# Optimization experiments

Measured on AMD Instinct MI355X. Metric: run time of the kernel, lower is better.

The kernel has to match this reference:

```python
import jax, jax.numpy as jnp
import numpy as np

N_NODES = 50000
N_EDGES = 1600000
IN_DIM = 128
HEADS = 4
OUT_DIM = 32
LEAKY_SLOPE = 0.2
BETA = 0.5
C = 1.2


def setup_inputs() -> dict:
    key = jax.random.key(0)
    k1, k2, k3, k4, k5, k6 = jax.random.split(key, 6)
    x = jax.random.normal(k1, (N_NODES, IN_DIM), dtype=jnp.float32)
    edge_index = jax.random.randint(k2, (2, N_EDGES), 0, N_NODES, dtype=jnp.int64)
    # GATConv params: shared linear (no bias), per-head attention vectors, output bias
    glorot = 1.0 / np.sqrt(IN_DIM)
    W = jax.random.uniform(k3, (IN_DIM, HEADS * OUT_DIM), jnp.float32, -glorot, glorot)
    att_src = jax.random.uniform(k4, (HEADS, OUT_DIM), jnp.float32, -glorot, glorot)
    att_dst = jax.random.uniform(k5, (HEADS, OUT_DIM), jnp.float32, -glorot, glorot)
    bias = jnp.zeros((HEADS * OUT_DIM,), jnp.float32)
    return {"x": x, "edge_index": edge_index, "W": W,
            "att_src": att_src, "att_dst": att_dst, "bias": bias}


def reference(x, edge_index, W, att_src, att_dst, bias):
    N = x.shape[0]
    H, D = att_src.shape
    # add self loops (edge j->i aggregates at i)
    loop = jnp.arange(N, dtype=edge_index.dtype)
    src = jnp.concatenate([edge_index[0], loop])  # [Etot]
    dst = jnp.concatenate([edge_index[1], loop])
    # per-head projection
    xp = (x @ W).reshape(N, H, D)                 # [N,H,D]
    a_src = jnp.einsum('nhd,hd->nh', xp, att_src)  # [N,H]
    a_dst = jnp.einsum('nhd,hd->nh', xp, att_dst)
    alpha = jax.nn.leaky_relu(a_src[src] + a_dst[dst], LEAKY_SLOPE)  # [Etot,H]
    # scatter-softmax over incoming edges per target node (self loops ensure coverage)
    amax = jax.ops.segment_max(alpha, dst, num_segments=N)
    e = jnp.exp(alpha - amax[dst])
    denom = jax.ops.segment_sum(e, dst, num_segments=N)
    w = e / (denom[dst] + 1e-16)                  # [Etot,H]
    # weighted scatter-add aggregation
    msg = xp[src] * w[:, :, None]                 # [Etot,H,D]
    out = jax.ops.segment_sum(msg, dst, num_segments=N).reshape(N, H * D)
    z = out + bias
    # beta-mix Swish (non-learnable swish beta = 1)
    return BETA * z + (C - BETA) * (z * jax.nn.sigmoid(z))
```

## Files before the change

kernel.cpp:

```cpp
#include <hip/hip_runtime.h>
#include <hip/hip_bf16.h>
#include <hip/hip_fp16.h>
#include <stdint.h>

#define LEAKY 0.2f
#define MIX_BETA 0.5f
#define MIX_C 1.2f

#define FBITS 7
#define FSZ   (1 << FBITS)
#define NBMX  512
#define CH    4096
#define EPT   16
#define CAPP  5632

using short8 = __attribute__((ext_vector_type(8))) short;
using f32x4  = __attribute__((ext_vector_type(4))) float;

__device__ __forceinline__ unsigned f2bf(float f) {
    unsigned u = __float_as_uint(f);
    return (u + 0x7fffu + ((u >> 16) & 1u)) >> 16;
}
__device__ __forceinline__ unsigned pack2bf(float a, float b) {
    return f2bf(a) | (f2bf(b) << 16);
}
__device__ __forceinline__ float hlo(unsigned u) {
    return __half2float(__ushort_as_half((uint16_t)(u & 0xFFFFu)));
}
__device__ __forceinline__ float hhi(unsigned u) {
    return __half2float(__ushort_as_half((uint16_t)(u >> 16)));
}
__device__ __forceinline__ float leaky_exp(float v) {
    v = fmaxf(v, LEAKY * v);
    return __expf(v);
}

__global__ __launch_bounds__(512) void k_prep(const void* x, const void* ei, const void* W,
                                              const void* att_s, const void* att_d,
                                              const void* bias, int N, int* flags,
                                              float* att_sf, float* att_df, float* biasf,
                                              uint16_t* Wtg, int* gbcursor) {
    __shared__ uint16_t wt[128][136];
    __shared__ int lf[2];
    const int t = threadIdx.x;
    if (t < NBMX) gbcursor[t] = 0;
    if (t < 64) {
        const uint16_t* u = (const uint16_t*)x;
        uint16_t v = u[2 * t];
        int ef = (v >> 7) & 0xFF;
        bool ok = (ef >= 90 && ef <= 140);
        unsigned long long all_ok = __ballot(ok);
        const unsigned long long* e64 = (const unsigned long long*)ei;
        bool big = (e64[t] >= (unsigned long long)N);
        unsigned long long anybig = __ballot(big);
        if (t == 0) {
            int f0 = (all_ok == ~0ull) ? 1 : 0;
            int f1 = (anybig != 0ull) ? 1 : 0;
            flags[0] = f0; flags[1] = f1;
            lf[0] = f0; lf[1] = f1;
        }
    }
    __syncthreads();
    const bool bf = lf[0] != 0;
    if (t >= 64 && t < 448) {
        int i = t - 64;
        const void* in; float* out; int idx;
        if (i < 128)      { in = att_s; out = att_sf; idx = i; }
        else if (i < 256) { in = att_d; out = att_df; idx = i - 128; }
        else              { in = bias;  out = biasf;  idx = i - 256; }
        float v = bf ? __uint_as_float(((unsigned)((const uint16_t*)in)[idx]) << 16)
                     : ((const float*)in)[idx];
        out[idx] = v;
    }
    for (int s = t; s < 4096; s += 512) {
        int k = s >> 5, c4 = (s & 31) * 4;
        ushort4 hv;
        if (bf) {
            hv = *(const ushort4*)((const uint16_t*)W + k * 128 + c4);
        } else {
            float4 v = *(const float4*)((const float*)W + k * 128 + c4);
            hv.x = (uint16_t)f2bf(v.x); hv.y = (uint16_t)f2bf(v.y);
            hv.z = (uint16_t)f2bf(v.z); hv.w = (uint16_t)f2bf(v.w);
        }
        wt[c4 + 0][k] = hv.x; wt[c4 + 1][k] = hv.y;
        wt[c4 + 2][k] = hv.z; wt[c4 + 3][k] = hv.w;
    }
    __syncthreads();
    for (int s = t; s < 2048; s += 512) {
        int r = s >> 4, ch = (s & 15) * 8;
        *(int4*)(Wtg + r * 128 + ch) = *(const int4*)&wt[r][ch];
    }
}

__global__ __launch_bounds__(256) void k_mid(const void* x, const void* ei,
                                             const uint16_t* Wtg,
                                             const float* att_sf, const float* att_df,
                                             const int* flags, int N, int E, int G,
                                             int nb, int cap, int* gbcursor,
                                             unsigned* entries,
                                             unsigned* xph, float* a_src, float* a_dst) {
    __shared__ char smem[40960] __attribute__((aligned(16)));
    const int t = threadIdx.x;

    if ((int)blockIdx.x < G) {
        uint16_t (*xs)[136]  = (uint16_t(*)[136])smem;
        float (*asrc_t)[4]   = (float(*)[4])(smem + 34816);
        float (*adst_t)[4]   = (float(*)[4])(smem + 36864);
        const bool bf = flags[0] != 0;
        const int row0 = blockIdx.x * 128;

        for (int s = t; s < 4096; s += 256) {
            int r = s >> 5, kc = (s & 31) * 4;
            int rr = row0 + r; if (rr >= N) rr = N - 1;
            size_t g = (size_t)rr * 128 + kc;
            ushort4 hv;
            if (bf) {
                hv = *(const ushort4*)((const uint16_t*)x + g);
            } else {
                float4 v = *(const float4*)((const float*)x + g);
                hv.x = (uint16_t)f2bf(v.x); hv.y = (uint16_t)f2bf(v.y);
                hv.z = (uint16_t)f2bf(v.z); hv.w = (uint16_t)f2bf(v.w);
            }
            *(ushort4*)&xs[r][kc] = hv;
        }
        __syncthreads();

        const int w = t >> 6, l = t & 63;
        const int rA = l & 15;
        const int kg = (l >> 4) * 8;
        f32x4 acc[2][8];
#pragma unroll
        for (int fr = 0; fr < 2; ++fr)
#pragma unroll
            for (int fc = 0; fc < 8; ++fc) acc[fr][fc] = (f32x4){0.f, 0.f, 0.f, 0.f};

#pragma unroll
        for (int kk = 0; kk < 4; ++kk) {
            const int kb = kk * 32 + kg;
            short8 a0 = *(const short8*)&xs[w * 32 + rA][kb];
            short8 a1 = *(const short8*)&xs[w * 32 + 16 + rA][kb];
            const uint16_t* wp = Wtg + rA * 128 + kb;
#pragma unroll
            for (int fc = 0; fc < 8; ++fc) {
                short8 b = *(const short8*)(wp + fc * 2048);
                acc[0][fc] = __builtin_amdgcn_mfma_f32_16x16x32_bf16(a0, b, acc[0][fc], 0, 0, 0);
                acc[1][fc] = __builtin_amdgcn_mfma_f32_16x16x32_bf16(a1, b, acc[1][fc], 0, 0, 0);
            }
        }
        __syncthreads();

#pragma unroll
        for (int fr = 0; fr < 2; ++fr)
#pragma unroll
            for (int fc = 0; fc < 8; ++fc) {
                int row = w * 32 + fr * 16 + (l >> 4) * 4;
                int col = fc * 16 + rA;
#pragma unroll
                for (int j = 0; j < 4; ++j)
                    xs[row + j][col] = __half_as_ushort(__float2half(acc[fr][fc][j]));
            }
        __syncthreads();

        for (int s = t; s < 2048; s += 256) {
            int r = s >> 4, ch = (s & 15) * 8;
            int rr = row0 + r;
            if (rr < N)
                *(int4*)((uint16_t*)xph + (size_t)rr * 128 + ch) = *(const int4*)&xs[r][ch];
        }
        for (int s = t; s < 512; s += 256) {
            int r = s >> 2, hh = s & 3;
            int rr = row0 + r;
            if (rr < N) {
                float ss = 0.f, sd = 0.f;
#pragma unroll
                for (int q = 0; q < 32; ++q) {
                    float v = __half2float(__ushort_as_half(xs[r][hh * 32 + q]));
                    ss = fmaf(v, att_sf[hh * 32 + q], ss);
                    sd = fmaf(v, att_df[hh * 32 + q], sd);
                }
                a_src[(size_t)rr * 4 + hh] = ss;
                a_dst[(size_t)rr * 4 + hh] = sd;
            }
        }
    } else {
        unsigned* st  = (unsigned*)smem;
        uint16_t* bb  = (uint16_t*)(smem + 16384);
        int* lcnt     = (int*)(smem + 24576);
        int* loff     = (int*)(smem + 26624);
        int* lbase    = (int*)(smem + 28672);
        int* wcur     = (int*)(smem + 30720);
        int* sc       = (int*)(smem + 32768);
        const bool is32 = flags[1] != 0;
        const int chunk0 = ((int)blockIdx.x - G) * CH;
        const int nvalid = min(CH, E - chunk0);

        int se[EPT], de[EPT];
        lcnt[t] = 0; lcnt[t + 256] = 0;
        wcur[t] = 0; wcur[t + 256] = 0;
        __syncthreads();
#pragma unroll
        for (int k = 0; k < EPT; ++k) {
            int i = chunk0 + k * 256 + t;
            if (i < E) {
                int s, d;
                if (is32) { const int* p = (const int*)ei; s = p[i]; d = p[E + i]; }
                else { const long long* p = (const long long*)ei; s = (int)p[i]; d = (int)p[E + i]; }
                se[k] = s; de[k] = d;
                atomicAdd(&lcnt[d >> FBITS], 1);
            } else {
                de[k] = -1;
            }
        }
        __syncthreads();
        sc[t] = lcnt[2 * t] + lcnt[2 * t + 1];
        __syncthreads();
        for (int o = 1; o < 256; o <<= 1) {
            int v = (t >= o) ? sc[t - o] : 0;
            __syncthreads();
            sc[t] += v;
            __syncthreads();
        }
        {
            int excl = (t > 0) ? sc[t - 1] : 0;
            int k0 = 2 * t, k1 = 2 * t + 1;
            loff[k0] = excl;
            loff[k1] = excl + lcnt[k0];
#pragma unroll
            for (int q = 0; q < 2; ++q) {
                int k = k0 + q;
                if (k < nb && lcnt[k]) {
                    int m = min(lcnt[k], cap);
                    int base = atomicAdd(&gbcursor[k], lcnt[k]);
                    if (base > cap - m) base = cap - m;
                    if (base < 0) base = 0;
                    lbase[k] = base;
                }
            }
        }
        __syncthreads();
#pragma unroll
        for (int k = 0; k < EPT; ++k) {
            int d = de[k];
            if (d >= 0) {
                int b = d >> FBITS;
                int slot = atomicAdd(&wcur[b], 1);
                int pos = loff[b] + slot;
                st[pos] = (unsigned)se[k] | ((unsigned)(d & (FSZ - 1)) << 17);
                bb[pos] = (uint16_t)b;
            }
        }
        __syncthreads();
        for (int s = t; s < nvalid; s += 256) {
            int b = bb[s];
            int pos = lbase[b] + (s - loff[b]);
            if (pos >= 0 && pos < cap)
                entries[(size_t)b * cap + pos] = st[s];
        }
    }
}

__global__ __launch_bounds__(1024) void k_final(const unsigned* entries, const int* gbcursor,
                                                int cap, int N,
                                                const float* a_src, const float* a_dst,
                                                const unsigned* xph, const float* biasf,
                                                const int* flags, void* out) {
    __shared__ uint16_t ssrc_l[CAPP];
    __shared__ __half   ews_l[(CAPP / 4) * 16];
    __shared__ int ncnt[FSZ], nscan[FSZ], wcur[FSZ], poff[FSZ];
    const int b = blockIdx.x;
    const int t = threadIdx.x;
    const int node0 = b << FBITS;
    const size_t eb = (size_t)b * cap;
    const int count = min(gbcursor[b], cap);

    for (int i = t; i < CAPP / 2; i += 1024) ((unsigned*)ssrc_l)[i] = 0u;
    for (int i = t; i < (CAPP / 4) * 8; i += 1024) ((unsigned*)ews_l)[i] = 0u;
    if (t < FSZ) ncnt[t] = 0;
    __syncthreads();
    for (int i = t; i < count; i += 1024)
        atomicAdd(&ncnt[entries[eb + i] >> 17], 1);
    __syncthreads();
    if (t < FSZ) nscan[t] = (ncnt[t] + 3) & ~3;
    __syncthreads();
    for (int o = 1; o < FSZ; o <<= 1) {
        int v = (t < FSZ && t >= o) ? nscan[t - o] : 0;
        __syncthreads();
        if (t < FSZ) nscan[t] += v;
        __syncthreads();
    }
    if (t < FSZ) {
        int pcnt = (ncnt[t] + 3) & ~3;
        int px = nscan[t] - pcnt;
        wcur[t] = px;
        poff[t] = px;
    }
    __syncthreads();
    for (int i = t; i < count; i += 1024) {
        unsigned e = entries[eb + i];
        int dlo = (int)(e >> 17);
        int s = (int)(e & 0x1FFFFu);
        int slot = atomicAdd(&wcur[dlo], 1);
        if (slot < CAPP) {
            int d = node0 + dlo;
            float4 as = *(const float4*)(a_src + (size_t)s * 4);
            float4 ad = *(const float4*)(a_dst + (size_t)d * 4);
            float e0 = leaky_exp(as.x + ad.x);
            float e1 = leaky_exp(as.y + ad.y);
            float e2 = leaky_exp(as.z + ad.z);
            float e3 = leaky_exp(as.w + ad.w);
            ssrc_l[slot] = (uint16_t)s;
            __half* pe = &ews_l[(slot >> 2) * 16];
            int j = slot & 3;
            pe[j]      = __float2half(e0);
            pe[4 + j]  = __float2half(e1);
            pe[8 + j]  = __float2half(e2);
            pe[12 + j] = __float2half(e3);
        }
    }
    __syncthreads();

    const int wv = t >> 6, lane = t & 63;
    const int hi = lane >> 5;
    const int l = lane & 31;
    const int d0 = l * 4;
    const int h = l >> 3;
    const char* xb = (const char*)xph;
    const int outbf = flags[0];

    for (int k = wv; k < FSZ / 2; k += 16) {
        int ln = 2 * k + hi;
        int n = node0 + ln;
        bool ok = n < N;
        int nn = ok ? n : (N - 1);
        int nc = ok ? ncnt[ln] : 0;

        float adst = a_dst[(size_t)nn * 4 + h];
        float e = leaky_exp(a_src[(size_t)nn * 4 + h] + adst);
        uint2 xw = *(const uint2*)(xb + (size_t)nn * 256 + d0 * 2);
        float4 acc;
        acc.x = e * hlo(xw.x); acc.y = e * hhi(xw.x);
        acc.z = e * hlo(xw.y); acc.w = e * hhi(xw.y);
        float den = e;

        const int beg = ok ? poff[ln] : 0;
        const int gb = beg >> 2;
        const int ng = (nc + 3) >> 2;
        int g = 0;
        for (; g + 2 <= ng; g += 2) {
            ushort4 s4a = *(const ushort4*)&ssrc_l[beg + 4 * g];
            ushort4 s4b = *(const ushort4*)&ssrc_l[beg + 4 * g + 4];
            uint2 ea = *(const uint2*)&ews_l[(gb + g) * 16 + h * 4];
            uint2 ebw = *(const uint2*)&ews_l[(gb + g + 1) * 16 + h * 4];
            uint2 w0 = *(const uint2*)(xb + (size_t)s4a.x * 256 + d0 * 2);
            uint2 w1 = *(const uint2*)(xb + (size_t)s4a.y * 256 + d0 * 2);
            uint2 w2 = *(const uint2*)(xb + (size_t)s4a.z * 256 + d0 * 2);
            uint2 w3 = *(const uint2*)(xb + (size_t)s4a.w * 256 + d0 * 2);
            uint2 w4 = *(const uint2*)(xb + (size_t)s4b.x * 256 + d0 * 2);
            uint2 w5 = *(const uint2*)(xb + (size_t)s4b.y * 256 + d0 * 2);
            uint2 w6 = *(const uint2*)(xb + (size_t)s4b.z * 256 + d0 * 2);
            uint2 w7 = *(const uint2*)(xb + (size_t)s4b.w * 256 + d0 * 2);
            float e0 = hlo(ea.x), e1 = hhi(ea.x), e2 = hlo(ea.y), e3 = hhi(ea.y);
            float e4 = hlo(ebw.x), e5 = hhi(ebw.x), e6 = hlo(ebw.y), e7 = hhi(ebw.y);
            acc.x = fmaf(e0, hlo(w0.x), acc.x); acc.y = fmaf(e0, hhi(w0.x), acc.y);
            acc.z = fmaf(e0, hlo(w0.y), acc.z); acc.w = fmaf(e0, hhi(w0.y), acc.w);
            acc.x = fmaf(e1, hlo(w1.x), acc.x); acc.y = fmaf(e1, hhi(w1.x), acc.y);
            acc.z = fmaf(e1, hlo(w1.y), acc.z); acc.w = fmaf(e1, hhi(w1.y), acc.w);
            acc.x = fmaf(e2, hlo(w2.x), acc.x); acc.y = fmaf(e2, hhi(w2.x), acc.y);
            acc.z = fmaf(e2, hlo(w2.y), acc.z); acc.w = fmaf(e2, hhi(w2.y), acc.w);
            acc.x = fmaf(e3, hlo(w3.x), acc.x); acc.y = fmaf(e3, hhi(w3.x), acc.y);
            acc.z = fmaf(e3, hlo(w3.y), acc.z); acc.w = fmaf(e3, hhi(w3.y), acc.w);
            acc.x = fmaf(e4, hlo(w4.x), acc.x); acc.y = fmaf(e4, hhi(w4.x), acc.y);
            acc.z = fmaf(e4, hlo(w4.y), acc.z); acc.w = fmaf(e4, hhi(w4.y), acc.w);
            acc.x = fmaf(e5, hlo(w5.x), acc.x); acc.y = fmaf(e5, hhi(w5.x), acc.y);
            acc.z = fmaf(e5, hlo(w5.y), acc.z); acc.w = fmaf(e5, hhi(w5.y), acc.w);
            acc.x = fmaf(e6, hlo(w6.x), acc.x); acc.y = fmaf(e6, hhi(w6.x), acc.y);
            acc.z = fmaf(e6, hlo(w6.y), acc.z); acc.w = fmaf(e6, hhi(w6.y), acc.w);
            acc.x = fmaf(e7, hlo(w7.x), acc.x); acc.y = fmaf(e7, hhi(w7.x), acc.y);
            acc.z = fmaf(e7, hlo(w7.y), acc.z); acc.w = fmaf(e7, hhi(w7.y), acc.w);
            den += ((e0 + e1) + (e2 + e3)) + ((e4 + e5) + (e6 + e7));
        }
        if (g < ng) {
            ushort4 s4 = *(const ushort4*)&ssrc_l[beg + 4 * g];
            uint2 ea = *(const uint2*)&ews_l[(gb + g) * 16 + h * 4];
            float e0 = hlo(ea.x), e1 = hhi(ea.x), e2 = hlo(ea.y), e3 = hhi(ea.y);
            uint2 w0 = *(const uint2*)(xb + (size_t)s4.x * 256 + d0 * 2);
            uint2 w1 = *(const uint2*)(xb + (size_t)s4.y * 256 + d0 * 2);
            uint2 w2 = *(const uint2*)(xb + (size_t)s4.z * 256 + d0 * 2);
            uint2 w3 = *(const uint2*)(xb + (size_t)s4.w * 256 + d0 * 2);
            acc.x = fmaf(e0, hlo(w0.x), acc.x); acc.y = fmaf(e0, hhi(w0.x), acc.y);
            acc.z = fmaf(e0, hlo(w0.y), acc.z); acc.w = fmaf(e0, hhi(w0.y), acc.w);
            acc.x = fmaf(e1, hlo(w1.x), acc.x); acc.y = fmaf(e1, hhi(w1.x), acc.y);
            acc.z = fmaf(e1, hlo(w1.y), acc.z); acc.w = fmaf(e1, hhi(w1.y), acc.w);
            acc.x = fmaf(e2, hlo(w2.x), acc.x); acc.y = fmaf(e2, hhi(w2.x), acc.y);
            acc.z = fmaf(e2, hlo(w2.y), acc.z); acc.w = fmaf(e2, hhi(w2.y), acc.w);
            acc.x = fmaf(e3, hlo(w3.x), acc.x); acc.y = fmaf(e3, hhi(w3.x), acc.y);
            acc.z = fmaf(e3, hlo(w3.y), acc.z); acc.w = fmaf(e3, hhi(w3.y), acc.w);
            den += (e0 + e1) + (e2 + e3);
        }
        float inv = 1.f / (den + 1e-16f);
        float4 bv = *(const float4*)(biasf + d0);
        float z0 = fmaf(acc.x, inv, bv.x);
        float z1 = fmaf(acc.y, inv, bv.y);
        float z2 = fmaf(acc.z, inv, bv.z);
        float z3 = fmaf(acc.w, inv, bv.w);
        float r0 = MIX_BETA * z0 + (MIX_C - MIX_BETA) * z0 / (1.f + __expf(-z0));
        float r1 = MIX_BETA * z1 + (MIX_C - MIX_BETA) * z1 / (1.f + __expf(-z1));
        float r2 = MIX_BETA * z2 + (MIX_C - MIX_BETA) * z2 / (1.f + __expf(-z2));
        float r3 = MIX_BETA * z3 + (MIX_C - MIX_BETA) * z3 / (1.f + __expf(-z3));
        if (ok) {
            if (outbf) {
                uint2 ov = make_uint2(pack2bf(r0, r1), pack2bf(r2, r3));
                *(uint2*)((uint16_t*)out + (size_t)n * 128 + d0) = ov;
            } else {
                *(float4*)((float*)out + (size_t)n * 128 + d0) = make_float4(r0, r1, r2, r3);
            }
        }
    }
}

extern "C" void kernel_launch(void* const* d_in, const int* in_sizes, int n_in,
                              void* d_out, int out_size, void* d_ws, size_t ws_size,
                              hipStream_t stream) {
    const void* x     = d_in[0];
    const void* ei    = d_in[1];
    const void* W     = d_in[2];
    const void* att_s = d_in[3];
    const void* att_d = d_in[4];
    const void* bias  = d_in[5];
    const int N = in_sizes[0] / 128;
    const int E = in_sizes[1] / 2;
    const int NB = (N + FSZ - 1) >> FBITS;
    int cap = E / NB + E / (8 * NB) + 512;
    const int capmax = CAPP - 3 * FSZ - 8;
    if (cap > capmax) cap = capmax;

    char* ws = (char*)d_ws;
    size_t off = 0;
    auto alloc = [&](size_t bytes) -> void* {
        void* p = ws + off;
        off += (bytes + 255) & ~(size_t)255;
        return p;
    };
    int* flags        = (int*)alloc(16);
    unsigned* entries = (unsigned*)alloc((size_t)NB * cap * 4);
    int* gbcursor     = (int*)alloc(NBMX * 4);
    unsigned* xph     = (unsigned*)alloc((size_t)N * 64 * 4);
    float* a_src      = (float*)alloc((size_t)N * 4 * 4);
    float* a_dst      = (float*)alloc((size_t)N * 4 * 4);
    float* att_sf     = (float*)alloc(128 * 4);
    float* att_df     = (float*)alloc(128 * 4);
    float* biasf      = (float*)alloc(128 * 4);
    uint16_t* Wtg     = (uint16_t*)alloc(128 * 128 * 2);

    const int G = (N + 127) / 128;
    const int S = (E + CH - 1) / CH;

    k_prep<<<1, 512, 0, stream>>>(x, ei, W, att_s, att_d, bias, N, flags,
                                  att_sf, att_df, biasf, Wtg, gbcursor);
    k_mid<<<G + S, 256, 0, stream>>>(x, ei, Wtg, att_sf, att_df, flags, N, E, G,
                                     NB, cap, gbcursor, entries, xph, a_src, a_dst);
    k_final<<<NB, 1024, 0, stream>>>(entries, gbcursor, cap, N, a_src, a_dst,
                                     xph, biasf, flags, d_out);
}
```

Measured before the change: 118.2 us.

## Halve destination bucket size and streamline final aggregation kernel staging

Destination buckets shrink from 128 to 64 nodes, so there are twice as many buckets. The edge-binning chunk and per-thread edge counts shrink to match, and the local scan now handles four buckets per thread. The final kernel runs 512 threads per block and caches a_dst for the bucket in shared memory. It keeps its edge entries in registers instead of reading them from global memory twice, and it zeroes only the padding slots rather than the whole shared buffers. The aim is more blocks for better GPU fill and less redundant global and shared-memory traffic, at the cost of more global atomics on bucket cursors and tighter per-bucket capacity margins.

Measured after the change: 138.1 us. 1.17x slower.

```diff
diff --git a/kernel.cpp b/kernel.cpp
--- a/kernel.cpp
+++ b/kernel.cpp
@@ -7,12 +7,12 @@
 #define MIX_BETA 0.5f
 #define MIX_C 1.2f
 
-#define FBITS 7
+#define FBITS 6
 #define FSZ   (1 << FBITS)
-#define NBMX  512
-#define CH    4096
-#define EPT   16
-#define CAPP  5632
+#define NBMX  1024
+#define CH    3072
+#define EPT   12
+#define CAPP  2944
 
 using short8 = __attribute__((ext_vector_type(8))) short;
 using f32x4  = __attribute__((ext_vector_type(4))) float;
@@ -43,7 +43,7 @@
     __shared__ uint16_t wt[128][136];
     __shared__ int lf[2];
     const int t = threadIdx.x;
-    if (t < NBMX) gbcursor[t] = 0;
+    gbcursor[t] = 0; gbcursor[t + 512] = 0;
     if (t < 64) {
         const uint16_t* u = (const uint16_t*)x;
         uint16_t v = u[2 * t];
@@ -99,13 +99,11 @@
                                              int nb, int cap, int* gbcursor,
                                              unsigned* entries,
                                              unsigned* xph, float* a_src, float* a_dst) {
-    __shared__ char smem[40960] __attribute__((aligned(16)));
+    __shared__ char smem[35840] __attribute__((aligned(16)));
     const int t = threadIdx.x;
 
     if ((int)blockIdx.x < G) {
-        uint16_t (*xs)[136]  = (uint16_t(*)[136])smem;
-        float (*asrc_t)[4]   = (float(*)[4])(smem + 34816);
-        float (*adst_t)[4]   = (float(*)[4])(smem + 36864);
+        uint16_t (*xs)[136] = (uint16_t(*)[136])smem;
         const bool bf = flags[0] != 0;
         const int row0 = blockIdx.x * 128;
 
@@ -184,19 +182,19 @@
         }
     } else {
         unsigned* st  = (unsigned*)smem;
-        uint16_t* bb  = (uint16_t*)(smem + 16384);
-        int* lcnt     = (int*)(smem + 24576);
-        int* loff     = (int*)(smem + 26624);
-        int* lbase    = (int*)(smem + 28672);
+        uint16_t* bb  = (uint16_t*)(smem + 12288);
+        int* lcnt     = (int*)(smem + 18432);
+        int* loff     = (int*)(smem + 22528);
+        int* lbase    = (int*)(smem + 26624);
         int* wcur     = (int*)(smem + 30720);
-        int* sc       = (int*)(smem + 32768);
+        int* sc       = (int*)(smem + 34816);
         const bool is32 = flags[1] != 0;
         const int chunk0 = ((int)blockIdx.x - G) * CH;
         const int nvalid = min(CH, E - chunk0);
 
         int se[EPT], de[EPT];
-        lcnt[t] = 0; lcnt[t + 256] = 0;
-        wcur[t] = 0; wcur[t + 256] = 0;
+#pragma unroll
+        for (int q = 0; q < 4; ++q) { lcnt[t + 256 * q] = 0; wcur[t + 256 * q] = 0; }
         __syncthreads();
 #pragma unroll
         for (int k = 0; k < EPT; ++k) {
@@ -212,7 +210,8 @@
             }
         }
         __syncthreads();
-        sc[t] = lcnt[2 * t] + lcnt[2 * t + 1];
+        int c0 = lcnt[4 * t], c1 = lcnt[4 * t + 1], c2 = lcnt[4 * t + 2], c3 = lcnt[4 * t + 3];
+        sc[t] = c0 + c1 + c2 + c3;
         __syncthreads();
         for (int o = 1; o < 256; o <<= 1) {
             int v = (t >= o) ? sc[t - o] : 0;
@@ -221,16 +220,16 @@
             __syncthreads();
         }
         {
-            int excl = (t > 0) ? sc[t - 1] : 0;
-            int k0 = 2 * t, k1 = 2 * t + 1;
-            loff[k0] = excl;
-            loff[k1] = excl + lcnt[k0];
-#pragma unroll
-            for (int q = 0; q < 2; ++q) {
-                int k = k0 + q;
-                if (k < nb && lcnt[k]) {
-                    int m = min(lcnt[k], cap);
-                    int base = atomicAdd(&gbcursor[k], lcnt[k]);
+            int base0 = sc[t] - (c0 + c1 + c2 + c3);
+            int off4[4] = {base0, base0 + c0, base0 + c0 + c1, base0 + c0 + c1 + c2};
+            int cnt4[4] = {c0, c1, c2, c3};
+#pragma unroll
+            for (int q = 0; q < 4; ++q) {
+                int k = 4 * t + q;
+                loff[k] = off4[q];
+                if (k < nb && cnt4[q]) {
+                    int m = min(cnt4[q], cap);
+                    int base = atomicAdd(&gbcursor[k], cnt4[q]);
                     if (base > cap - m) base = cap - m;
                     if (base < 0) base = 0;
                     lbase[k] = base;
@@ -259,26 +258,35 @@
     }
 }
 
-__global__ __launch_bounds__(1024) void k_final(const unsigned* entries, const int* gbcursor,
-                                                int cap, int N,
-                                                const float* a_src, const float* a_dst,
-                                                const unsigned* xph, const float* biasf,
-                                                const int* flags, void* out) {
+__global__ __launch_bounds__(512) void k_final(const unsigned* entries, const int* gbcursor,
+                                               int cap, int N,
+                                               const float* a_src, const float* a_dst,
+                                               const unsigned* xph, const float* biasf,
+                                               const int* flags, void* out) {
     __shared__ uint16_t ssrc_l[CAPP];
     __shared__ __half   ews_l[(CAPP / 4) * 16];
     __shared__ int ncnt[FSZ], nscan[FSZ], wcur[FSZ], poff[FSZ];
+    __shared__ float adst_l[FSZ][4];
     const int b = blockIdx.x;
     const int t = threadIdx.x;
     const int node0 = b << FBITS;
     const size_t eb = (size_t)b * cap;
     const int count = min(gbcursor[b], cap);
 
-    for (int i = t; i < CAPP / 2; i += 1024) ((unsigned*)ssrc_l)[i] = 0u;
-    for (int i = t; i < (CAPP / 4) * 8; i += 1024) ((unsigned*)ews_l)[i] = 0u;
+    if (t < FSZ * 4) {
+        int ln = t >> 2, hh = t & 3;
+        int n = node0 + ln;
+        adst_l[ln][hh] = (n < N) ? a_dst[(size_t)n * 4 + hh] : 0.f;
+    }
     if (t < FSZ) ncnt[t] = 0;
     __syncthreads();
-    for (int i = t; i < count; i += 1024)
-        atomicAdd(&ncnt[entries[eb + i] >> 17], 1);
+    unsigned er[6];
+    int nr = 0;
+    for (int i = t; i < count; i += 512) {
+        unsigned e = entries[eb + i];
+        er[nr++] = e;
+        atomicAdd(&ncnt[e >> 17], 1);
+    }
     __syncthreads();
     if (t < FSZ) nscan[t] = (ncnt[t] + 3) & ~3;
     __syncthreads();
@@ -295,19 +303,31 @@
         poff[t] = px;
     }
     __syncthreads();
-    for (int i = t; i < count; i += 1024) {
-        unsigned e = entries[eb + i];
+    if (t < FSZ) {
+        int c = ncnt[t];
+        int pcnt = (c + 3) & ~3;
+        int px = poff[t];
+        for (int p = c; p < pcnt; ++p) {
+            int slot = px + p;
+            ssrc_l[slot] = 0;
+            __half* pe = &ews_l[(slot >> 2) * 16];
+            int j = slot & 3;
+            const __half z = __float2half(0.f);
+            pe[j] = z; pe[4 + j] = z; pe[8 + j] = z; pe[12 + j] = z;
+        }
+    }
+    for (int r = 0; r < nr; ++r) {
+        unsigned e = er[r];
         int dlo = (int)(e >> 17);
         int s = (int)(e & 0x1FFFFu);
         int slot = atomicAdd(&wcur[dlo], 1);
         if (slot < CAPP) {
-            int d = node0 + dlo;
             float4 as = *(const float4*)(a_src + (size_t)s * 4);
-            float4 ad = *(const float4*)(a_dst + (size_t)d * 4);
-            float e0 = leaky_exp(as.x + ad.x);
-            float e1 = leaky_exp(as.y + ad.y);
-            float e2 = leaky_exp(as.z + ad.z);
-            float e3 = leaky_exp(as.w + ad.w);
+            const float* ad = adst_l[dlo];
+            float e0 = leaky_exp(as.x + ad[0]);
+            float e1 = leaky_exp(as.y + ad[1]);
+            float e2 = leaky_exp(as.z + ad[2]);
+            float e3 = leaky_exp(as.w + ad[3]);
             ssrc_l[slot] = (uint16_t)s;
             __half* pe = &ews_l[(slot >> 2) * 16];
             int j = slot & 3;
@@ -327,14 +347,14 @@
     const char* xb = (const char*)xph;
     const int outbf = flags[0];
 
-    for (int k = wv; k < FSZ / 2; k += 16) {
+    for (int k = wv; k < FSZ / 2; k += 8) {
         int ln = 2 * k + hi;
         int n = node0 + ln;
         bool ok = n < N;
         int nn = ok ? n : (N - 1);
         int nc = ok ? ncnt[ln] : 0;
 
-        float adst = a_dst[(size_t)nn * 4 + h];
+        float adst = adst_l[ok ? ln : 0][h];
         float e = leaky_exp(a_src[(size_t)nn * 4 + h] + adst);
         uint2 xw = *(const uint2*)(xb + (size_t)nn * 256 + d0 * 2);
         float4 acc;
@@ -430,7 +450,7 @@
     const int N = in_sizes[0] / 128;
     const int E = in_sizes[1] / 2;
     const int NB = (N + FSZ - 1) >> FBITS;
-    int cap = E / NB + E / (8 * NB) + 512;
+    int cap = E / NB + E / (8 * NB) + 256;
     const int capmax = CAPP - 3 * FSZ - 8;
     if (cap > capmax) cap = capmax;
 
@@ -459,6 +479,6 @@
                                   att_sf, att_df, biasf, Wtg, gbcursor);
     k_mid<<<G + S, 256, 0, stream>>>(x, ei, Wtg, att_sf, att_df, flags, N, E, G,
                                      NB, cap, gbcursor, entries, xph, a_src, a_dst);
-    k_final<<<NB, 1024, 0, stream>>>(entries, gbcursor, cap, N, a_src, a_dst,
-                                     xph, biasf, flags, d_out);
-}
+    k_final<<<NB, 512, 0, stream>>>(entries, gbcursor, cap, N, a_src, a_dst,
+                                    xph, biasf, flags, d_out);
+}
```

## Precompute attention logits via folded W·att and move edge exp into scatter

Applied to the files above, without the earlier changes.

Folds the attention vectors into the weight matrix (W·att_src, W·att_dst), so a new multi-block prep kernel computes a_src/a_dst straight from x before the GEMM/bucketing kernel. The edge-bucketing blocks can then compute the leaky-exp weights at scatter time and write them, packed as half, to a new global array next to the edge metadata. This drops the shared-memory staging buffer and the second scatter pass. The final kernel no longer recomputes exponentials and zeroes only the padding slots. The cost is extra global traffic for the per-edge weight array and a second read of x in the prep kernel. Logits are now computed in fp32 from x rather than from the half-rounded projection.

Result: slower. 196.1 us (+65.9%).

```diff
diff --git a/kernel.cpp b/kernel.cpp
--- a/kernel.cpp
+++ b/kernel.cpp
@@ -13,6 +13,7 @@
 #define CH    4096
 #define EPT   16
 #define CAPP  5632
+#define PREROWS 512
 
 using short8 = __attribute__((ext_vector_type(8))) short;
 using f32x4  = __attribute__((ext_vector_type(4))) float;
@@ -24,6 +25,10 @@
 __device__ __forceinline__ unsigned pack2bf(float a, float b) {
     return f2bf(a) | (f2bf(b) << 16);
 }
+__device__ __forceinline__ unsigned pack2h(float a, float b) {
+    return (unsigned)__half_as_ushort(__float2half(a)) |
+           ((unsigned)__half_as_ushort(__float2half(b)) << 16);
+}
 __device__ __forceinline__ float hlo(unsigned u) {
     return __half2float(__ushort_as_half((uint16_t)(u & 0xFFFFu)));
 }
@@ -34,78 +39,137 @@
     v = fmaxf(v, LEAKY * v);
     return __expf(v);
 }
-
-__global__ __launch_bounds__(512) void k_prep(const void* x, const void* ei, const void* W,
-                                              const void* att_s, const void* att_d,
-                                              const void* bias, int N, int* flags,
-                                              float* att_sf, float* att_df, float* biasf,
-                                              uint16_t* Wtg, int* gbcursor) {
+__device__ __forceinline__ float4 ld4f(const void* p, size_t idx, bool bf) {
+    if (bf) {
+        ushort4 q = *(const ushort4*)((const uint16_t*)p + idx);
+        float4 v;
+        v.x = __uint_as_float((unsigned)q.x << 16);
+        v.y = __uint_as_float((unsigned)q.y << 16);
+        v.z = __uint_as_float((unsigned)q.z << 16);
+        v.w = __uint_as_float((unsigned)q.w << 16);
+        return v;
+    }
+    return *(const float4*)((const float*)p + idx);
+}
+
+__global__ __launch_bounds__(256) void k_pre(const void* x, const void* ei, const void* W,
+                                             const void* att_s, const void* att_d,
+                                             const void* bias, int N, int* flags,
+                                             float* biasf, uint16_t* Wtg, int* gbcursor,
+                                             float* a_src, float* a_dst) {
     __shared__ uint16_t wt[128][136];
+    __shared__ float vsd[128][8];
     __shared__ int lf[2];
     const int t = threadIdx.x;
-    if (t < NBMX) gbcursor[t] = 0;
+    const int b = blockIdx.x;
+
     if (t < 64) {
         const uint16_t* u = (const uint16_t*)x;
         uint16_t v = u[2 * t];
         int ef = (v >> 7) & 0xFF;
-        bool ok = (ef >= 90 && ef <= 140);
-        unsigned long long all_ok = __ballot(ok);
+        bool okb = (ef >= 90 && ef <= 140);
+        unsigned long long all_ok = __ballot(okb);
         const unsigned long long* e64 = (const unsigned long long*)ei;
         bool big = (e64[t] >= (unsigned long long)N);
         unsigned long long anybig = __ballot(big);
         if (t == 0) {
-            int f0 = (all_ok == ~0ull) ? 1 : 0;
-            int f1 = (anybig != 0ull) ? 1 : 0;
-            flags[0] = f0; flags[1] = f1;
-            lf[0] = f0; lf[1] = f1;
-        }
-    }
+            lf[0] = (all_ok == ~0ull) ? 1 : 0;
+            lf[1] = (anybig != 0ull) ? 1 : 0;
+            if (b == 0) { flags[0] = lf[0]; flags[1] = lf[1]; }
+        }
+    }
+    if (b == 0) { gbcursor[t] = 0; gbcursor[t + 256] = 0; }
     __syncthreads();
     const bool bf = lf[0] != 0;
-    if (t >= 64 && t < 448) {
-        int i = t - 64;
-        const void* in; float* out; int idx;
-        if (i < 128)      { in = att_s; out = att_sf; idx = i; }
-        else if (i < 256) { in = att_d; out = att_df; idx = i - 128; }
-        else              { in = bias;  out = biasf;  idx = i - 256; }
-        float v = bf ? __uint_as_float(((unsigned)((const uint16_t*)in)[idx]) << 16)
-                     : ((const float*)in)[idx];
-        out[idx] = v;
-    }
-    for (int s = t; s < 4096; s += 512) {
-        int k = s >> 5, c4 = (s & 31) * 4;
-        ushort4 hv;
-        if (bf) {
-            hv = *(const ushort4*)((const uint16_t*)W + k * 128 + c4);
-        } else {
-            float4 v = *(const float4*)((const float*)W + k * 128 + c4);
-            hv.x = (uint16_t)f2bf(v.x); hv.y = (uint16_t)f2bf(v.y);
-            hv.z = (uint16_t)f2bf(v.z); hv.w = (uint16_t)f2bf(v.w);
-        }
-        wt[c4 + 0][k] = hv.x; wt[c4 + 1][k] = hv.y;
-        wt[c4 + 2][k] = hv.z; wt[c4 + 3][k] = hv.w;
-    }
-    __syncthreads();
-    for (int s = t; s < 2048; s += 512) {
-        int r = s >> 4, ch = (s & 15) * 8;
-        *(int4*)(Wtg + r * 128 + ch) = *(const int4*)&wt[r][ch];
+
+    if (t < 128) {
+        float vs[4] = {0.f, 0.f, 0.f, 0.f}, vd[4] = {0.f, 0.f, 0.f, 0.f};
+        for (int c4 = 0; c4 < 32; ++c4) {
+            float4 wv  = ld4f(W, (size_t)t * 128 + c4 * 4, bf);
+            float4 as4 = ld4f(att_s, (size_t)c4 * 4, bf);
+            float4 ad4 = ld4f(att_d, (size_t)c4 * 4, bf);
+            int h = c4 >> 3;
+            vs[h] = fmaf(wv.x, as4.x, vs[h]); vs[h] = fmaf(wv.y, as4.y, vs[h]);
+            vs[h] = fmaf(wv.z, as4.z, vs[h]); vs[h] = fmaf(wv.w, as4.w, vs[h]);
+            vd[h] = fmaf(wv.x, ad4.x, vd[h]); vd[h] = fmaf(wv.y, ad4.y, vd[h]);
+            vd[h] = fmaf(wv.z, ad4.z, vd[h]); vd[h] = fmaf(wv.w, ad4.w, vd[h]);
+        }
+#pragma unroll
+        for (int h = 0; h < 4; ++h) { vsd[t][h] = vs[h]; vsd[t][4 + h] = vd[h]; }
+    }
+    if (b == 0 && t >= 128 && t < 256) {
+        int i2 = t - 128;
+        biasf[i2] = bf ? __uint_as_float(((unsigned)((const uint16_t*)bias)[i2]) << 16)
+                       : ((const float*)bias)[i2];
+    }
+    if (b == 0) {
+        for (int s = t; s < 4096; s += 256) {
+            int k = s >> 5, c4 = (s & 31) * 4;
+            ushort4 hv;
+            if (bf) {
+                hv = *(const ushort4*)((const uint16_t*)W + k * 128 + c4);
+            } else {
+                float4 v = *(const float4*)((const float*)W + k * 128 + c4);
+                hv.x = (uint16_t)f2bf(v.x); hv.y = (uint16_t)f2bf(v.y);
+                hv.z = (uint16_t)f2bf(v.z); hv.w = (uint16_t)f2bf(v.w);
+            }
+            wt[c4 + 0][k] = hv.x; wt[c4 + 1][k] = hv.y;
+            wt[c4 + 2][k] = hv.z; wt[c4 + 3][k] = hv.w;
+        }
+    }
+    __syncthreads();
+    if (b == 0) {
+        for (int s = t; s < 2048; s += 256) {
+            int r = s >> 4, ch = (s & 15) * 8;
+            *(int4*)(Wtg + r * 128 + ch) = *(const int4*)&wt[r][ch];
+        }
+    }
+
+    const int wv = t >> 6, lane = t & 63, hi = lane >> 5, l = lane & 31;
+    float vreg[4][8];
+#pragma unroll
+    for (int q = 0; q < 4; ++q) {
+        float4 v0 = *(const float4*)&vsd[l * 4 + q][0];
+        float4 v1 = *(const float4*)&vsd[l * 4 + q][4];
+        vreg[q][0] = v0.x; vreg[q][1] = v0.y; vreg[q][2] = v0.z; vreg[q][3] = v0.w;
+        vreg[q][4] = v1.x; vreg[q][5] = v1.y; vreg[q][6] = v1.z; vreg[q][7] = v1.w;
+    }
+    const int base = b * PREROWS + wv * (PREROWS / 4);
+    for (int it = 0; it < PREROWS / 8; ++it) {
+        int r = base + it * 2 + hi;
+        bool okr = r < N;
+        int rr = okr ? r : (N - 1);
+        float4 xv = ld4f(x, (size_t)rr * 128 + l * 4, bf);
+        float acc[8];
+#pragma unroll
+        for (int j = 0; j < 8; ++j) {
+            float v = xv.x * vreg[0][j];
+            v = fmaf(xv.y, vreg[1][j], v);
+            v = fmaf(xv.z, vreg[2][j], v);
+            v = fmaf(xv.w, vreg[3][j], v);
+            v += __shfl_xor(v, 1, 32); v += __shfl_xor(v, 2, 32);
+            v += __shfl_xor(v, 4, 32); v += __shfl_xor(v, 8, 32);
+            v += __shfl_xor(v, 16, 32);
+            acc[j] = v;
+        }
+        if (l == 0 && okr) {
+            *(float4*)(a_src + (size_t)r * 4) = make_float4(acc[0], acc[1], acc[2], acc[3]);
+            *(float4*)(a_dst + (size_t)r * 4) = make_float4(acc[4], acc[5], acc[6], acc[7]);
+        }
     }
 }
 
 __global__ __launch_bounds__(256) void k_mid(const void* x, const void* ei,
                                              const uint16_t* Wtg,
-                                             const float* att_sf, const float* att_df,
+                                             const float* a_src, const float* a_dst,
                                              const int* flags, int N, int E, int G,
                                              int nb, int cap, int* gbcursor,
-                                             unsigned* entries,
-                                             unsigned* xph, float* a_src, float* a_dst) {
-    __shared__ char smem[40960] __attribute__((aligned(16)));
+                                             unsigned* emeta, uint2* ew, unsigned* xph) {
+    __shared__ char smem[34816] __attribute__((aligned(16)));
     const int t = threadIdx.x;
 
     if ((int)blockIdx.x < G) {
-        uint16_t (*xs)[136]  = (uint16_t(*)[136])smem;
-        float (*asrc_t)[4]   = (float(*)[4])(smem + 34816);
-        float (*adst_t)[4]   = (float(*)[4])(smem + 36864);
+        uint16_t (*xs)[136] = (uint16_t(*)[136])smem;
         const bool bf = flags[0] != 0;
         const int row0 = blockIdx.x * 128;
 
@@ -142,9 +206,9 @@
             const uint16_t* wp = Wtg + rA * 128 + kb;
 #pragma unroll
             for (int fc = 0; fc < 8; ++fc) {
-                short8 b = *(const short8*)(wp + fc * 2048);
-                acc[0][fc] = __builtin_amdgcn_mfma_f32_16x16x32_bf16(a0, b, acc[0][fc], 0, 0, 0);
-                acc[1][fc] = __builtin_amdgcn_mfma_f32_16x16x32_bf16(a1, b, acc[1][fc], 0, 0, 0);
+                short8 bfr = *(const short8*)(wp + fc * 2048);
+                acc[0][fc] = __builtin_amdgcn_mfma_f32_16x16x32_bf16(a0, bfr, acc[0][fc], 0, 0, 0);
+                acc[1][fc] = __builtin_amdgcn_mfma_f32_16x16x32_bf16(a1, bfr, acc[1][fc], 0, 0, 0);
             }
         }
         __syncthreads();
@@ -167,32 +231,14 @@
             if (rr < N)
                 *(int4*)((uint16_t*)xph + (size_t)rr * 128 + ch) = *(const int4*)&xs[r][ch];
         }
-        for (int s = t; s < 512; s += 256) {
-            int r = s >> 2, hh = s & 3;
-            int rr = row0 + r;
-            if (rr < N) {
-                float ss = 0.f, sd = 0.f;
-#pragma unroll
-                for (int q = 0; q < 32; ++q) {
-                    float v = __half2float(__ushort_as_half(xs[r][hh * 32 + q]));
-                    ss = fmaf(v, att_sf[hh * 32 + q], ss);
-                    sd = fmaf(v, att_df[hh * 32 + q], sd);
-                }
-                a_src[(size_t)rr * 4 + hh] = ss;
-                a_dst[(size_t)rr * 4 + hh] = sd;
-            }
-        }
     } else {
-        unsigned* st  = (unsigned*)smem;
-        uint16_t* bb  = (uint16_t*)(smem + 16384);
-        int* lcnt     = (int*)(smem + 24576);
-        int* loff     = (int*)(smem + 26624);
-        int* lbase    = (int*)(smem + 28672);
-        int* wcur     = (int*)(smem + 30720);
-        int* sc       = (int*)(smem + 32768);
+        int* lcnt  = (int*)smem;
+        int* loff  = (int*)(smem + 2048);
+        int* lbase = (int*)(smem + 4096);
+        int* wcur  = (int*)(smem + 6144);
+        int* sc    = (int*)(smem + 8192);
         const bool is32 = flags[1] != 0;
         const int chunk0 = ((int)blockIdx.x - G) * CH;
-        const int nvalid = min(CH, E - chunk0);
 
         int se[EPT], de[EPT];
         lcnt[t] = 0; lcnt[t + 256] = 0;
@@ -212,7 +258,8 @@
             }
         }
         __syncthreads();
-        sc[t] = lcnt[2 * t] + lcnt[2 * t + 1];
+        int c0 = lcnt[2 * t], c1 = lcnt[2 * t + 1];
+        sc[t] = c0 + c1;
         __syncthreads();
         for (int o = 1; o < 256; o <<= 1) {
             int v = (t >= o) ? sc[t - o] : 0;
@@ -221,16 +268,17 @@
             __syncthreads();
         }
         {
-            int excl = (t > 0) ? sc[t - 1] : 0;
+            int excl = sc[t] - (c0 + c1);
             int k0 = 2 * t, k1 = 2 * t + 1;
             loff[k0] = excl;
-            loff[k1] = excl + lcnt[k0];
+            loff[k1] = excl + c0;
+            int cnt2[2] = {c0, c1};
 #pragma unroll
             for (int q = 0; q < 2; ++q) {
                 int k = k0 + q;
-                if (k < nb && lcnt[k]) {
-                    int m = min(lcnt[k], cap);
-                    int base = atomicAdd(&gbcursor[k], lcnt[k]);
+                if (k < nb && cnt2[q]) {
+                    int m = min(cnt2[q], cap);
+                    int base = atomicAdd(&gbcursor[k], cnt2[q]);
                     if (base > cap - m) base = cap - m;
                     if (base < 0) base = 0;
                     lbase[k] = base;
@@ -242,25 +290,28 @@
         for (int k = 0; k < EPT; ++k) {
             int d = de[k];
             if (d >= 0) {
-                int b = d >> FBITS;
-                int slot = atomicAdd(&wcur[b], 1);
-                int pos = loff[b] + slot;
-                st[pos] = (unsigned)se[k] | ((unsigned)(d & (FSZ - 1)) << 17);
-                bb[pos] = (uint16_t)b;
-            }
-        }
-        __syncthreads();
-        for (int s = t; s < nvalid; s += 256) {
-            int b = bb[s];
-            int pos = lbase[b] + (s - loff[b]);
-            if (pos >= 0 && pos < cap)
-                entries[(size_t)b * cap + pos] = st[s];
-        }
-    }
-}
-
-__global__ __launch_bounds__(1024) void k_final(const unsigned* entries, const int* gbcursor,
-                                                int cap, int N,
+                int s = se[k];
+                int bk = d >> FBITS;
+                int slot = atomicAdd(&wcur[bk], 1);
+                int pos = lbase[bk] + slot;
+                if (pos < cap) {
+                    float4 as = *(const float4*)(a_src + (size_t)s * 4);
+                    float4 ad = *(const float4*)(a_dst + (size_t)d * 4);
+                    float e0 = leaky_exp(as.x + ad.x);
+                    float e1 = leaky_exp(as.y + ad.y);
+                    float e2 = leaky_exp(as.z + ad.z);
+                    float e3 = leaky_exp(as.w + ad.w);
+                    size_t gi = (size_t)bk * cap + pos;
+                    emeta[gi] = (unsigned)s | ((unsigned)(d & (FSZ - 1)) << 17);
+                    ew[gi] = make_uint2(pack2h(e0, e1), pack2h(e2, e3));
+                }
+            }
+        }
+    }
+}
+
+__global__ __launch_bounds__(1024) void k_final(const unsigned* emeta, const uint2* ew,
+                                                const int* gbcursor, int cap, int N,
                                                 const float* a_src, const float* a_dst,
                                                 const unsigned* xph, const float* biasf,
                                                 const int* flags, void* out) {
@@ -273,12 +324,15 @@
     const size_t eb = (size_t)b * cap;
     const int count = min(gbcursor[b], cap);
 
-    for (int i = t; i < CAPP / 2; i += 1024) ((unsigned*)ssrc_l)[i] = 0u;
-    for (int i = t; i < (CAPP / 4) * 8; i += 1024) ((unsigned*)ews_l)[i] = 0u;
     if (t < FSZ) ncnt[t] = 0;
     __syncthreads();
-    for (int i = t; i < count; i += 1024)
-        atomicAdd(&ncnt[entries[eb + i] >> 17], 1);
+    unsigned er[6];
+    int nr = 0;
+    for (int i = t; i < count; i += 1024) {
+        unsigned e = emeta[eb + i];
+        er[nr++] = e;
+        atomicAdd(&ncnt[e >> 17], 1);
+    }
     __syncthreads();
     if (t < FSZ) nscan[t] = (ncnt[t] + 3) & ~3;
     __syncthreads();
@@ -295,26 +349,34 @@
         poff[t] = px;
     }
     __syncthreads();
-    for (int i = t; i < count; i += 1024) {
-        unsigned e = entries[eb + i];
+    if (t < FSZ) {
+        int c = ncnt[t];
+        int pcnt = (c + 3) & ~3;
+        int px = poff[t];
+        const __half z = __float2half(0.f);
+        for (int p = c; p < pcnt; ++p) {
+            int slot = px + p;
+            ssrc_l[slot] = 0;
+            __half* pe = &ews_l[(slot >> 2) * 16];
+            int j = slot & 3;
+            pe[j] = z; pe[4 + j] = z; pe[8 + j] = z; pe[12 + j] = z;
+        }
+    }
+    for (int r2 = 0; r2 < nr; ++r2) {
+        unsigned e = er[r2];
+        int i = t + r2 * 1024;
         int dlo = (int)(e >> 17);
         int s = (int)(e & 0x1FFFFu);
         int slot = atomicAdd(&wcur[dlo], 1);
         if (slot < CAPP) {
-            int d = node0 + dlo;
-            float4 as = *(const float4*)(a_src + (size_t)s * 4);
-            float4 ad = *(const float4*)(a_dst + (size_t)d * 4);
-            float e0 = leaky_exp(as.x + ad.x);
-            float e1 = leaky_exp(as.y + ad.y);
-            float e2 = leaky_exp(as.z + ad.z);
-            float e3 = leaky_exp(as.w + ad.w);
+            uint2 w = ew[eb + i];
             ssrc_l[slot] = (uint16_t)s;
             __half* pe = &ews_l[(slot >> 2) * 16];
             int j = slot & 3;
-            pe[j]      = __float2half(e0);
-            pe[4 + j]  = __float2half(e1);
-            pe[8 + j]  = __float2half(e2);
-            pe[12 + j] = __float2half(e3);
+            pe[j]      = __ushort_as_half((uint16_t)(w.x & 0xFFFFu));
+            pe[4 + j]  = __ushort_as_half((uint16_t)(w.x >> 16));
+            pe[8 + j]  = __ushort_as_half((uint16_t)(w.y & 0xFFFFu));
+            pe[12 + j] = __ushort_as_half((uint16_t)(w.y >> 16));
         }
     }
     __syncthreads();
@@ -442,23 +504,23 @@
         return p;
     };
     int* flags        = (int*)alloc(16);
-    unsigned* entries = (unsigned*)alloc((size_t)NB * cap * 4);
+    unsigned* emeta   = (unsigned*)alloc((size_t)NB * cap * 4);
+    uint2* ew         = (uint2*)alloc((size_t)NB * cap * 8);
     int* gbcursor     = (int*)alloc(NBMX * 4);
     unsigned* xph     = (unsigned*)alloc((size_t)N * 64 * 4);
     float* a_src      = (float*)alloc((size_t)N * 4 * 4);
     float* a_dst      = (float*)alloc((size_t)N * 4 * 4);
-    float* att_sf     = (float*)alloc(128 * 4);
-    float* att_df     = (float*)alloc(128 * 4);
     float* biasf      = (float*)alloc(128 * 4);
     uint16_t* Wtg     = (uint16_t*)alloc(128 * 128 * 2);
 
+    const int PB = (N + PREROWS - 1) / PREROWS;
     const int G = (N + 127) / 128;
     const int S = (E + CH - 1) / CH;
 
-    k_prep<<<1, 512, 0, stream>>>(x, ei, W, att_s, att_d, bias, N, flags,
-                                  att_sf, att_df, biasf, Wtg, gbcursor);
-    k_mid<<<G + S, 256, 0, stream>>>(x, ei, Wtg, att_sf, att_df, flags, N, E, G,
-                                     NB, cap, gbcursor, entries, xph, a_src, a_dst);
-    k_final<<<NB, 1024, 0, stream>>>(entries, gbcursor, cap, N, a_src, a_dst,
+    k_pre<<<PB, 256, 0, stream>>>(x, ei, W, att_s, att_d, bias, N, flags,
+                                  biasf, Wtg, gbcursor, a_src, a_dst);
+    k_mid<<<G + S, 256, 0, stream>>>(x, ei, Wtg, a_src, a_dst, flags, N, E, G,
+                                     NB, cap, gbcursor, emeta, ew, xph);
+    k_final<<<NB, 1024, 0, stream>>>(emeta, ew, gbcursor, cap, N, a_src, a_dst,
                                      xph, biasf, flags, d_out);
 }
```
